# Performance work log

Measured on AMD Instinct MI355X. Metric: run time of the kernel, lower is better.

The kernel has to match this reference:

```python
import jax, jax.numpy as jnp
import numpy as np
from jax import lax

K = 3           # dynamic-filter kernel size
NUM_TYPES = 216 # Qstr*Qcohe*Qangle = 3*3*24
C = 64          # in/out channels
GROUP = 4


def _conv(x, w, groups=1):
    return lax.conv_general_dilated(
        x, w, window_strides=(1, 1), padding='SAME',
        dimension_numbers=('NCHW', 'OIHW', 'NCHW'),
        feature_group_count=groups)


def setup_inputs() -> dict:
    key = jax.random.key(0)
    ks = jax.random.split(key, 7)
    B, H, W = 1, 64, 64
    x = jax.random.normal(ks[0], (B, C, H, W), dtype=jnp.float32)
    buckets = jax.random.randint(ks[1], (B, H, W), 0, NUM_TYPES)
    # body1: grouped 3x3 conv (in=out=64, groups=4 -> in/group=16)
    w1 = jax.random.normal(ks[2], (C, C // GROUP, 3, 3), dtype=jnp.float32) * 0.05
    b1 = jax.random.normal(ks[3], (C,), dtype=jnp.float32) * 0.05
    # filter embedding: one flattened (out, in*K*K + bias) filter per bucket type
    emb = jax.random.normal(ks[4], (NUM_TYPES, C * (C * K * K + 1)), dtype=jnp.float32) * 0.1
    # body2: 1x1 conv
    w2 = jax.random.normal(ks[5], (C, C, 1, 1), dtype=jnp.float32) * 0.05
    b2 = jax.random.normal(ks[6], (C,), dtype=jnp.float32) * 0.05
    return {'x': x, 'buckets': buckets, 'w1': w1, 'b1': b1, 'emb': emb, 'w2': w2, 'b2': b2}


def reference(x, buckets, w1, b1, emb, w2, b2):
    B, Cin, H, W = x.shape
    Cout = w2.shape[0]
    ckk = emb.shape[1] // Cout - 1  # in*K*K
    # body1: grouped conv + ReLU
    h = jax.nn.relu(_conv(x, w1, groups=GROUP) + b1[None, :, None, None])
    # per-pixel bucket-indexed dynamic conv
    patches = lax.conv_general_dilated_patches(
        h, (K, K), (1, 1), 'SAME',
        dimension_numbers=('NCHW', 'OIHW', 'NCHW'))  # [B, Cin*K*K, H, W]
    f = emb[buckets].reshape(B, H, W, Cout, ckk + 1)   # gathered per-pixel filters
    out = jnp.einsum('bchw,bhwoc->bohw', patches, f[..., :-1])
    out = out + jnp.transpose(f[..., -1], (0, 3, 1, 2))  # per-pixel bias
    # body2: ReLU -> 1x1 conv
    out = _conv(jax.nn.relu(out), w2) + b2[None, :, None, None]
    # residual + ReLU
    return jax.nn.relu(out + x)
```

## Files before the change

### kernel.cpp

```cpp
#include <hip/hip_runtime.h>

#define NTYPES 216
#define NPIX   4096
#define KD     576
#define ROWLEN 577
#define NPC    32
#define PSTR   640

typedef __attribute__((ext_vector_type(8))) short short8;
typedef __attribute__((ext_vector_type(4))) float f32x4;
typedef __attribute__((ext_vector_type(4), aligned(4))) float f32x4u;
typedef __attribute__((ext_vector_type(8))) unsigned short u16x8;
typedef __attribute__((ext_vector_type(4))) unsigned short u16x4;

static __device__ __forceinline__ unsigned short f2bf(float f) {
    unsigned u = __builtin_bit_cast(unsigned, f);
    unsigned r = (u + 0x7FFFu + ((u >> 16) & 1u)) >> 16;
    return (unsigned short)r;
}

__global__ __launch_bounds__(256) void prep_kernel(
        const float* __restrict__ x, const float* __restrict__ w1,
        const float* __restrict__ b1, const int* __restrict__ buckets,
        unsigned short* __restrict__ hbf, int* __restrict__ offsets,
        int* __restrict__ sorted) {
    int tid = threadIdx.x;
    if (blockIdx.x == 256) {
        __shared__ int cnt[256];
        __shared__ int pre[256];
        cnt[tid] = 0;
        __syncthreads();
        for (int i = tid; i < NPIX; i += 256) atomicAdd(&cnt[buckets[i]], 1);
        __syncthreads();
        int v = cnt[tid];
        pre[tid] = v;
        __syncthreads();
        #pragma unroll
        for (int s = 1; s < 256; s <<= 1) {
            int add = (tid >= s) ? pre[tid - s] : 0;
            __syncthreads();
            pre[tid] += add;
            __syncthreads();
        }
        int excl = pre[tid] - v;
        if (tid <= NTYPES) offsets[tid] = excl;
        cnt[tid] = excl;
        __syncthreads();
        for (int i = tid; i < NPIX; i += 256) {
            int b = buckets[i];
            sorted[atomicAdd(&cnt[b], 1)] = i;
        }
        return;
    }
    int flat = blockIdx.x * 256 + tid;
    int x4 = flat & 15;
    int y  = (flat >> 4) & 63;
    int c  = flat >> 10;
    int g  = c >> 4;
    const float* wrow = w1 + c * 144;
    float o0, o1, o2, o3;
    o0 = o1 = o2 = o3 = b1[c];
    #pragma unroll
    for (int ci = 0; ci < 16; ++ci) {
        const float* xp = x + (g * 16 + ci) * 4096;
        #pragma unroll
        for (int dy = 0; dy < 3; ++dy) {
            int yy = y + dy - 1;
            if (yy < 0 || yy > 63) continue;
            const float* row = xp + yy * 64 + x4 * 4;
            f32x4 mm = *(const f32x4*)row;
            float xl = (x4 > 0)  ? row[-1] : 0.f;
            float xr = (x4 < 15) ? row[4]  : 0.f;
            float wa = wrow[ci * 9 + dy * 3 + 0];
            float wb = wrow[ci * 9 + dy * 3 + 1];
            float wc = wrow[ci * 9 + dy * 3 + 2];
            o0 = fmaf(wa, xl,    fmaf(wb, mm[0], fmaf(wc, mm[1], o0)));
            o1 = fmaf(wa, mm[0], fmaf(wb, mm[1], fmaf(wc, mm[2], o1)));
            o2 = fmaf(wa, mm[1], fmaf(wb, mm[2], fmaf(wc, mm[3], o2)));
            o3 = fmaf(wa, mm[2], fmaf(wb, mm[3], fmaf(wc, xr,    o3)));
        }
    }
    int pix0 = y * 64 + x4 * 4;
    hbf[(pix0 + 0) * 64 + c] = f2bf(fmaxf(o0, 0.f));
    hbf[(pix0 + 1) * 64 + c] = f2bf(fmaxf(o1, 0.f));
    hbf[(pix0 + 2) * 64 + c] = f2bf(fmaxf(o2, 0.f));
    hbf[(pix0 + 3) * 64 + c] = f2bf(fmaxf(o3, 0.f));
}

__global__ __launch_bounds__(512) void dyn_kernel(
        const unsigned short* __restrict__ hbf, const float* __restrict__ emb,
        const float* __restrict__ w2, const float* __restrict__ b2,
        const float* __restrict__ x, const int* __restrict__ offsets,
        const int* __restrict__ sorted, float* __restrict__ out) {

    __shared__ alignas(16) unsigned short Wl[64 * PSTR];
    __shared__ alignas(16) unsigned short Pl[NPC * PSTR];
    __shared__ alignas(16) unsigned short Dl[NPC * 72];
    __shared__ alignas(16) unsigned short w2l[64 * 72];
    __shared__ float bias_l[64];
    __shared__ int pixs[NPC];

    int t = blockIdx.x;
    int start = offsets[t];
    int n = offsets[t + 1] - start;
    if (n <= 0) return;

    int tid  = threadIdx.x;
    int lane = tid & 63;
    int wv   = tid >> 6;
    int m    = wv & 3;
    int ph   = wv >> 2;
    int ra   = lane & 15;
    int kg   = lane >> 4;

    const float* eb = emb + (size_t)t * 36928;

    #pragma unroll
    for (int it = 0; it < 9; ++it) {
        int u  = tid + it * 512;
        int r  = u / 72;
        int c0 = (u - r * 72) * 8;
        const float* src = eb + r * ROWLEN + c0;
        f32x4u a = *(const f32x4u*)src;
        f32x4u b = *(const f32x4u*)(src + 4);
        unsigned short* wrow = &Wl[r * PSTR + (r & 7) * 8];
        #pragma unroll
        for (int j = 0; j < 8; ++j) {
            int c = c0 + j;
            int cch = c / 9, pos = c - cch * 9;
            float val = (j < 4) ? a[j] : b[j - 4];
            wrow[pos * 64 + cch] = f2bf(val);
        }
    }
    if (tid < 64) bias_l[tid] = eb[tid * ROWLEN + KD];

    {
        int o = tid >> 3, i8 = (tid & 7) * 8;
        const float* src = w2 + o * 64 + i8;
        u16x8 v;
        #pragma unroll
        for (int j = 0; j < 8; ++j) v[j] = f2bf(src[j]);
        *(u16x8*)&w2l[o * 72 + i8] = v;
    }
    __syncthreads();

    int rowW = m * 16 + ra;
    const unsigned short* pA = Wl + rowW * PSTR + (rowW & 7) * 8 + kg * 8;
    int ob0 = m * 16 + kg * 4;
    float bias0 = bias_l[ob0 + 0], bias1 = bias_l[ob0 + 1];
    float bias2 = bias_l[ob0 + 2], bias3 = bias_l[ob0 + 3];

    const unsigned short* pB = Pl + (ph * 16 + ra) * PSTR + (ra & 7) * 8 + kg * 8;

    int gp = tid >> 4;
    int gk = tid & 15;
    unsigned short* pdst = Pl + gp * PSTR + (gp & 7) * 8;

    for (int base = 0; base < n; base += NPC) {
        __syncthreads();
        if (tid < NPC) pixs[tid] = (base + tid < n) ? sorted[start + base + tid] : -1;
        __syncthreads();

        {
            int pixel = pixs[gp];
            int py = pixel >> 6, px = pixel & 63;
            #pragma unroll
            for (int dy = 0; dy < 3; ++dy) {
                int yy = py + dy - 1;
                bool yok = (yy >= 0 && yy < 64);
                #pragma unroll
                for (int dx = 0; dx < 3; ++dx) {
                    int pos = dy * 3 + dx;
                    int xx = px + dx - 1;
                    u16x4 v = {0, 0, 0, 0};
                    if (pixel >= 0 && yok && xx >= 0 && xx < 64)
                        v = *(const u16x4*)&hbf[(yy * 64 + xx) * 64 + gk * 4];
                    *(u16x4*)(pdst + pos * 64 + gk * 4) = v;
                }
            }
        }
        __syncthreads();

        f32x4 acc = {0.f, 0.f, 0.f, 0.f};
        #pragma unroll
        for (int ck = 0; ck < 9; ++ck) {
            #pragma unroll
            for (int ks = 0; ks < 2; ++ks) {
                u16x8 av = *(const u16x8*)(pA + ck * 64 + ks * 32);
                u16x8 bv = *(const u16x8*)(pB + ck * 64 + ks * 32);
                acc = __builtin_amdgcn_mfma_f32_16x16x32_bf16(
                          __builtin_bit_cast(short8, av),
                          __builtin_bit_cast(short8, bv), acc, 0, 0, 0);
            }
        }

        {
            int pi = ph * 16 + ra;
            u16x4 dv;
            dv[0] = f2bf(fmaxf(acc[0] + bias0, 0.f));
            dv[1] = f2bf(fmaxf(acc[1] + bias1, 0.f));
            dv[2] = f2bf(fmaxf(acc[2] + bias2, 0.f));
            dv[3] = f2bf(fmaxf(acc[3] + bias3, 0.f));
            *(u16x4*)&Dl[pi * 72 + ob0] = dv;
        }
        __syncthreads();

        f32x4 acc2 = {0.f, 0.f, 0.f, 0.f};
        #pragma unroll
        for (int ks = 0; ks < 2; ++ks) {
            u16x8 a2  = *(const u16x8*)&w2l[(m * 16 + ra) * 72 + ks * 32 + kg * 8];
            u16x8 b2v = *(const u16x8*)&Dl[(ph * 16 + ra) * 72 + ks * 32 + kg * 8];
            acc2 = __builtin_amdgcn_mfma_f32_16x16x32_bf16(
                       __builtin_bit_cast(short8, a2),
                       __builtin_bit_cast(short8, b2v), acc2, 0, 0, 0);
        }

        {
            int pi = ph * 16 + ra;
            int pixel = pixs[pi];
            if (pixel >= 0) {
                #pragma unroll
                for (int j = 0; j < 4; ++j) {
                    int o = ob0 + j;
                    float v = acc2[j] + b2[o] + x[o * 4096 + pixel];
                    out[o * 4096 + pixel] = fmaxf(v, 0.f);
                }
            }
        }
    }
}

extern "C" void kernel_launch(void* const* d_in, const int* in_sizes, int n_in,
                              void* d_out, int out_size, void* d_ws, size_t ws_size,
                              hipStream_t stream) {
    const float* x       = (const float*)d_in[0];
    const int*   buckets = (const int*)d_in[1];
    const float* w1      = (const float*)d_in[2];
    const float* b1      = (const float*)d_in[3];
    const float* emb     = (const float*)d_in[4];
    const float* w2      = (const float*)d_in[5];
    const float* b2      = (const float*)d_in[6];
    float* out = (float*)d_out;

    char* ws = (char*)d_ws;
    unsigned short* hbf = (unsigned short*)ws;
    int*   offsets      = (int*)(ws + (1 << 20));
    int*   sorted       = (int*)(ws + (1 << 20) + 4096);

    prep_kernel<<<257, 256, 0, stream>>>(x, w1, b1, buckets, hbf, offsets, sorted);
    dyn_kernel<<<NTYPES, 512, 0, stream>>>(hbf, emb, w2, b2, x, offsets, sorted, out);
}
```

Baseline: 33.92 us.

## Fuse prep and dynamic-filter kernels with a grid-wide done-counter handoff

Merges the grouped-conv prep kernel and the per-bucket dynamic-conv kernel into one launch. Each block now finds its own bucket's pixels by scanning the buckets array with a shared atomic counter, so the global counting sort is gone. The first 128 blocks also compute the bf16 hidden activations and signal completion through a release atomic that every block spin-waits on after staging its filter weights. This is meant to remove a kernel launch and the serial sort, and to overlap filter loading with the conv. In exchange it relies on all 216 blocks being co-resident, adds a memset, and caps each bucket at 160 pixels, which silently drops pixels for skewed bucket distributions.

```diff
diff --git a/kernel.cpp b/kernel.cpp
--- a/kernel.cpp
+++ b/kernel.cpp
@@ -6,6 +6,7 @@
 #define ROWLEN 577
 #define NPC    32
 #define PSTR   640
+#define MAXB   160
 
 typedef __attribute__((ext_vector_type(8))) short short8;
 typedef __attribute__((ext_vector_type(4))) float f32x4;
@@ -19,102 +20,79 @@
     return (unsigned short)r;
 }
 
-__global__ __launch_bounds__(256) void prep_kernel(
+__global__ __launch_bounds__(512) void fused_kernel(
         const float* __restrict__ x, const float* __restrict__ w1,
         const float* __restrict__ b1, const int* __restrict__ buckets,
-        unsigned short* __restrict__ hbf, int* __restrict__ offsets,
-        int* __restrict__ sorted) {
-    int tid = threadIdx.x;
-    if (blockIdx.x == 256) {
-        __shared__ int cnt[256];
-        __shared__ int pre[256];
-        cnt[tid] = 0;
-        __syncthreads();
-        for (int i = tid; i < NPIX; i += 256) atomicAdd(&cnt[buckets[i]], 1);
-        __syncthreads();
-        int v = cnt[tid];
-        pre[tid] = v;
-        __syncthreads();
-        #pragma unroll
-        for (int s = 1; s < 256; s <<= 1) {
-            int add = (tid >= s) ? pre[tid - s] : 0;
-            __syncthreads();
-            pre[tid] += add;
-            __syncthreads();
-        }
-        int excl = pre[tid] - v;
-        if (tid <= NTYPES) offsets[tid] = excl;
-        cnt[tid] = excl;
-        __syncthreads();
-        for (int i = tid; i < NPIX; i += 256) {
-            int b = buckets[i];
-            sorted[atomicAdd(&cnt[b], 1)] = i;
-        }
-        return;
-    }
-    int flat = blockIdx.x * 256 + tid;
-    int x4 = flat & 15;
-    int y  = (flat >> 4) & 63;
-    int c  = flat >> 10;
-    int g  = c >> 4;
-    const float* wrow = w1 + c * 144;
-    float o0, o1, o2, o3;
-    o0 = o1 = o2 = o3 = b1[c];
-    #pragma unroll
-    for (int ci = 0; ci < 16; ++ci) {
-        const float* xp = x + (g * 16 + ci) * 4096;
-        #pragma unroll
-        for (int dy = 0; dy < 3; ++dy) {
-            int yy = y + dy - 1;
-            if (yy < 0 || yy > 63) continue;
-            const float* row = xp + yy * 64 + x4 * 4;
-            f32x4 mm = *(const f32x4*)row;
-            float xl = (x4 > 0)  ? row[-1] : 0.f;
-            float xr = (x4 < 15) ? row[4]  : 0.f;
-            float wa = wrow[ci * 9 + dy * 3 + 0];
-            float wb = wrow[ci * 9 + dy * 3 + 1];
-            float wc = wrow[ci * 9 + dy * 3 + 2];
-            o0 = fmaf(wa, xl,    fmaf(wb, mm[0], fmaf(wc, mm[1], o0)));
-            o1 = fmaf(wa, mm[0], fmaf(wb, mm[1], fmaf(wc, mm[2], o1)));
-            o2 = fmaf(wa, mm[1], fmaf(wb, mm[2], fmaf(wc, mm[3], o2)));
-            o3 = fmaf(wa, mm[2], fmaf(wb, mm[3], fmaf(wc, xr,    o3)));
-        }
-    }
-    int pix0 = y * 64 + x4 * 4;
-    hbf[(pix0 + 0) * 64 + c] = f2bf(fmaxf(o0, 0.f));
-    hbf[(pix0 + 1) * 64 + c] = f2bf(fmaxf(o1, 0.f));
-    hbf[(pix0 + 2) * 64 + c] = f2bf(fmaxf(o2, 0.f));
-    hbf[(pix0 + 3) * 64 + c] = f2bf(fmaxf(o3, 0.f));
-}
-
-__global__ __launch_bounds__(512) void dyn_kernel(
-        const unsigned short* __restrict__ hbf, const float* __restrict__ emb,
-        const float* __restrict__ w2, const float* __restrict__ b2,
-        const float* __restrict__ x, const int* __restrict__ offsets,
-        const int* __restrict__ sorted, float* __restrict__ out) {
+        const float* __restrict__ emb, const float* __restrict__ w2,
+        const float* __restrict__ b2,
+        unsigned short* __restrict__ hbf, int* __restrict__ done,
+        float* __restrict__ out) {
 
     __shared__ alignas(16) unsigned short Wl[64 * PSTR];
     __shared__ alignas(16) unsigned short Pl[NPC * PSTR];
     __shared__ alignas(16) unsigned short Dl[NPC * 72];
     __shared__ alignas(16) unsigned short w2l[64 * 72];
     __shared__ float bias_l[64];
-    __shared__ int pixs[NPC];
-
-    int t = blockIdx.x;
-    int start = offsets[t];
-    int n = offsets[t + 1] - start;
-    if (n <= 0) return;
-
-    int tid  = threadIdx.x;
-    int lane = tid & 63;
-    int wv   = tid >> 6;
-    int m    = wv & 3;
-    int ph   = wv >> 2;
-    int ra   = lane & 15;
-    int kg   = lane >> 4;
-
-    const float* eb = emb + (size_t)t * 36928;
-
+    __shared__ int pixs[MAXB];
+    __shared__ int cnt_l;
+
+    int b   = blockIdx.x;
+    int tid = threadIdx.x;
+
+    if (tid == 0) cnt_l = 0;
+    __syncthreads();
+    {
+        int i0 = tid * 8;
+        int4 v0 = *(const int4*)&buckets[i0];
+        int4 v1 = *(const int4*)&buckets[i0 + 4];
+        int vv0 = v0.x, vv1 = v0.y, vv2 = v0.z, vv3 = v0.w;
+        int vv4 = v1.x, vv5 = v1.y, vv6 = v1.z, vv7 = v1.w;
+        #define SCAN1(VV, J) if ((VV) == b) { int p = atomicAdd(&cnt_l, 1); if (p < MAXB) pixs[p] = i0 + (J); }
+        SCAN1(vv0, 0) SCAN1(vv1, 1) SCAN1(vv2, 2) SCAN1(vv3, 3)
+        SCAN1(vv4, 4) SCAN1(vv5, 5) SCAN1(vv6, 6) SCAN1(vv7, 7)
+        #undef SCAN1
+    }
+
+    if (b < 128) {
+        int u  = b * 512 + tid;
+        int x4 = u & 15;
+        int y  = (u >> 4) & 63;
+        int c  = u >> 10;
+        int g  = c >> 4;
+        const float* wrow = w1 + c * 144;
+        float o0, o1, o2, o3;
+        o0 = o1 = o2 = o3 = b1[c];
+        #pragma unroll
+        for (int ci = 0; ci < 16; ++ci) {
+            const float* xp = x + (g * 16 + ci) * 4096;
+            #pragma unroll
+            for (int dy = 0; dy < 3; ++dy) {
+                int yy = y + dy - 1;
+                if (yy < 0 || yy > 63) continue;
+                const float* row = xp + yy * 64 + x4 * 4;
+                f32x4 mm = *(const f32x4*)row;
+                float xl = (x4 > 0)  ? row[-1] : 0.f;
+                float xr = (x4 < 15) ? row[4]  : 0.f;
+                float wa = wrow[ci * 9 + dy * 3 + 0];
+                float wb = wrow[ci * 9 + dy * 3 + 1];
+                float wc = wrow[ci * 9 + dy * 3 + 2];
+                o0 = fmaf(wa, xl,    fmaf(wb, mm[0], fmaf(wc, mm[1], o0)));
+                o1 = fmaf(wa, mm[0], fmaf(wb, mm[1], fmaf(wc, mm[2], o1)));
+                o2 = fmaf(wa, mm[1], fmaf(wb, mm[2], fmaf(wc, mm[3], o2)));
+                o3 = fmaf(wa, mm[2], fmaf(wb, mm[3], fmaf(wc, xr,    o3)));
+            }
+        }
+        int pix0 = y * 64 + x4 * 4;
+        hbf[(pix0 + 0) * 64 + c] = f2bf(fmaxf(o0, 0.f));
+        hbf[(pix0 + 1) * 64 + c] = f2bf(fmaxf(o1, 0.f));
+        hbf[(pix0 + 2) * 64 + c] = f2bf(fmaxf(o2, 0.f));
+        hbf[(pix0 + 3) * 64 + c] = f2bf(fmaxf(o3, 0.f));
+        __syncthreads();
+        if (tid == 0)
+            __hip_atomic_fetch_add(done, 1, __ATOMIC_RELEASE, __HIP_MEMORY_SCOPE_AGENT);
+    }
+
+    const float* eb = emb + (size_t)b * 36928;
     #pragma unroll
     for (int it = 0; it < 9; ++it) {
         int u  = tid + it * 512;
@@ -122,18 +100,17 @@
         int c0 = (u - r * 72) * 8;
         const float* src = eb + r * ROWLEN + c0;
         f32x4u a = *(const f32x4u*)src;
-        f32x4u b = *(const f32x4u*)(src + 4);
+        f32x4u bb = *(const f32x4u*)(src + 4);
         unsigned short* wrow = &Wl[r * PSTR + (r & 7) * 8];
         #pragma unroll
         for (int j = 0; j < 8; ++j) {
             int c = c0 + j;
             int cch = c / 9, pos = c - cch * 9;
-            float val = (j < 4) ? a[j] : b[j - 4];
+            float val = (j < 4) ? a[j] : bb[j - 4];
             wrow[pos * 64 + cch] = f2bf(val);
         }
     }
     if (tid < 64) bias_l[tid] = eb[tid * ROWLEN + KD];
-
     {
         int o = tid >> 3, i8 = (tid & 7) * 8;
         const float* src = w2 + o * 64 + i8;
@@ -142,14 +119,29 @@
         for (int j = 0; j < 8; ++j) v[j] = f2bf(src[j]);
         *(u16x8*)&w2l[o * 72 + i8] = v;
     }
+
+    if (tid == 0) {
+        while (__hip_atomic_load(done, __ATOMIC_ACQUIRE, __HIP_MEMORY_SCOPE_AGENT) < 128)
+            __builtin_amdgcn_s_sleep(2);
+        __threadfence();
+    }
     __syncthreads();
+
+    int n = cnt_l < MAXB ? cnt_l : MAXB;
+    if (n <= 0) return;
+
+    int lane = tid & 63;
+    int wv   = tid >> 6;
+    int m    = wv & 3;
+    int ph   = wv >> 2;
+    int ra   = lane & 15;
+    int kg   = lane >> 4;
 
     int rowW = m * 16 + ra;
     const unsigned short* pA = Wl + rowW * PSTR + (rowW & 7) * 8 + kg * 8;
     int ob0 = m * 16 + kg * 4;
     float bias0 = bias_l[ob0 + 0], bias1 = bias_l[ob0 + 1];
     float bias2 = bias_l[ob0 + 2], bias3 = bias_l[ob0 + 3];
-
     const unsigned short* pB = Pl + (ph * 16 + ra) * PSTR + (ra & 7) * 8 + kg * 8;
 
     int gp = tid >> 4;
@@ -157,13 +149,10 @@
     unsigned short* pdst = Pl + gp * PSTR + (gp & 7) * 8;
 
     for (int base = 0; base < n; base += NPC) {
-        __syncthreads();
-        if (tid < NPC) pixs[tid] = (base + tid < n) ? sorted[start + base + tid] : -1;
-        __syncthreads();
-
         {
-            int pixel = pixs[gp];
+            int pixel = (base + gp < n) ? pixs[base + gp] : -1;
             int py = pixel >> 6, px = pixel & 63;
+            u16x4 p0[9];
             #pragma unroll
             for (int dy = 0; dy < 3; ++dy) {
                 int yy = py + dy - 1;
@@ -175,9 +164,12 @@
                     u16x4 v = {0, 0, 0, 0};
                     if (pixel >= 0 && yok && xx >= 0 && xx < 64)
                         v = *(const u16x4*)&hbf[(yy * 64 + xx) * 64 + gk * 4];
-                    *(u16x4*)(pdst + pos * 64 + gk * 4) = v;
+                    p0[pos] = v;
                 }
             }
+            #pragma unroll
+            for (int pos = 0; pos < 9; ++pos)
+                *(u16x4*)(pdst + pos * 64 + gk * 4) = p0[pos];
         }
         __syncthreads();
 
@@ -217,7 +209,7 @@
 
         {
             int pi = ph * 16 + ra;
-            int pixel = pixs[pi];
+            int pixel = (base + pi < n) ? pixs[base + pi] : -1;
             if (pixel >= 0) {
                 #pragma unroll
                 for (int j = 0; j < 4; ++j) {
@@ -244,9 +236,9 @@
 
     char* ws = (char*)d_ws;
     unsigned short* hbf = (unsigned short*)ws;
-    int*   offsets      = (int*)(ws + (1 << 20));
-    int*   sorted       = (int*)(ws + (1 << 20) + 4096);
-
-    prep_kernel<<<257, 256, 0, stream>>>(x, w1, b1, buckets, hbf, offsets, sorted);
-    dyn_kernel<<<NTYPES, 512, 0, stream>>>(hbf, emb, w2, b2, x, offsets, sorted, out);
+    int* done           = (int*)(ws + (1 << 20));
+
+    hipMemsetAsync(done, 0, sizeof(int), stream);
+    fused_kernel<<<NTYPES, 512, 0, stream>>>(x, w1, b1, buckets, emb, w2, b2,
+                                             hbf, done, out);
 }
```

After: 77.46 us. 128% more time.
